# Kernel tuning notes

Hardware: AMD Instinct MI355X
Metric: run time of the kernel (lower is better)

## Reference

```python
import jax, jax.numpy as jnp
import numpy as np

H = 256  # hidden_dim
N = 100000  # num nodes in local_embedding
U = 65536  # num unary clauses
B = 65536  # num binary clauses


def setup_inputs() -> dict:
    key = jax.random.key(0)
    ks = jax.random.split(key, 20)
    s = 0.02
    inp = {
        "local_embedding": jax.random.normal(ks[0], (N, H), dtype=jnp.float32),
        "global_embedding": jax.random.normal(ks[1], (1, H), dtype=jnp.float32),
        "unary_idx": jax.random.randint(ks[2], (U, 2), 0, N, dtype=jnp.int64),
        "binary_idx": jax.random.randint(ks[3], (B, 3), 0, N, dtype=jnp.int64),
        # binary_op_layer: Linear(3H,2H) -> ReLU -> Linear(2H,H)
        "Wb1": jax.random.normal(ks[4], (3 * H, 2 * H), dtype=jnp.float32) * s,
        "bb1": jnp.zeros((2 * H,), dtype=jnp.float32),
        "Wb2": jax.random.normal(ks[5], (2 * H, H), dtype=jnp.float32) * s,
        "bb2": jnp.zeros((H,), dtype=jnp.float32),
        # ternary_op_layer: Linear(4H,2H) -> ReLU -> Linear(2H,H)
        "Wt1": jax.random.normal(ks[6], (4 * H, 2 * H), dtype=jnp.float32) * s,
        "bt1": jnp.zeros((2 * H,), dtype=jnp.float32),
        "Wt2": jax.random.normal(ks[7], (2 * H, H), dtype=jnp.float32) * s,
        "bt2": jnp.zeros((H,), dtype=jnp.float32),
        # common_layer: ReLU -> Linear(H,H) -> ReLU -> Linear(H,1)
        "Wc1": jax.random.normal(ks[8], (H, H), dtype=jnp.float32) * s,
        "bc1": jnp.zeros((H,), dtype=jnp.float32),
        "Wc2": jax.random.normal(ks[9], (H, 1), dtype=jnp.float32) * s,
        "bc2": jnp.zeros((1,), dtype=jnp.float32),
    }
    return inp


def _mlp_branch(rep, W1, b1, W2, b2, Wc1, bc1, Wc2, bc2):
    # op layer: Linear -> ReLU -> Linear
    h = jax.nn.relu(rep @ W1 + b1) @ W2 + b2  # [M, H]
    # common layer: ReLU -> Linear -> ReLU -> Linear(H,1)
    h = jax.nn.relu(jax.nn.relu(h) @ Wc1 + bc1) @ Wc2 + bc2  # [M, 1]
    return h[:, 0]


def reference(local_embedding, global_embedding, unary_idx, binary_idx,
              Wb1, bb1, Wb2, bb2, Wt1, bt1, Wt2, bt2, Wc1, bc1, Wc2, bc2):
    u = unary_idx.shape[0]
    b = binary_idx.shape[0]
    h = global_embedding.shape[-1]
    # gather [U,2,H] node embeddings, append global -> [U,3,H] -> [U,3H]
    g_u = jnp.broadcast_to(global_embedding[None, :, :], (u, 1, h))
    unary_rep = jnp.concatenate(
        (local_embedding[unary_idx, :], g_u), axis=1).reshape(u, 3 * h)
    x_u = _mlp_branch(unary_rep, Wb1, bb1, Wb2, bb2, Wc1, bc1, Wc2, bc2)
    # gather [B,3,H], append global -> [B,4,H] -> [B,4H]
    g_b = jnp.broadcast_to(global_embedding[None, :, :], (b, 1, h))
    binary_rep = jnp.concatenate(
        (local_embedding[binary_idx, :], g_b), axis=1).reshape(b, 4 * h)
    x_b = _mlp_branch(binary_rep, Wt1, bt1, Wt2, bt2, Wc1, bc1, Wc2, bc2)
    x = jnp.concatenate((x_u, x_b))
    return x.reshape(1, x.shape[-1])
```

## Files before the change

### kernel.cpp

```cpp
#include <hip/hip_runtime.h>
#include <cstdint>
#include <cstddef>

typedef __attribute__((ext_vector_type(8))) short s16x8;
typedef __attribute__((ext_vector_type(4))) float fx4;

#define AS1 __attribute__((address_space(1)))
#define AS3 __attribute__((address_space(3)))

__device__ __forceinline__ unsigned short f2bf(float f) {
    union { float f; unsigned u; } c; c.f = f;
    unsigned lsb = (c.u >> 16) & 1u;
    unsigned r = c.u + 0x7fffu + lsb;
    return (unsigned short)(r >> 16);
}

__global__ __launch_bounds__(256) void conv4(const float* __restrict__ src,
                                             unsigned short* __restrict__ dst, int n4) {
    int i = blockIdx.x * 256 + threadIdx.x;
    if (i >= n4) return;
    float4 v = reinterpret_cast<const float4*>(src)[i];
    ushort4 o;
    o.x = f2bf(v.x); o.y = f2bf(v.y); o.z = f2bf(v.z); o.w = f2bf(v.w);
    reinterpret_cast<ushort4*>(dst)[i] = o;
}

__global__ __launch_bounds__(256) void convT(const float* __restrict__ W,
                                             unsigned short* __restrict__ WT, int K, int N) {
    int i = blockIdx.x * 256 + threadIdx.x;
    if (i >= N * K) return;
    int n = i / K, k = i - n * K;
    WT[i] = f2bf(W[(size_t)k * N + n]);
}

__global__ __launch_bounds__(64) void foldbias(const float* __restrict__ g,
                                               const float* __restrict__ W1,
                                               const float* __restrict__ b1,
                                               float* __restrict__ bout,
                                               int K0, int N) {
    int n = blockIdx.x;
    int lane = threadIdx.x;
    float s = 0.f;
#pragma unroll
    for (int j = 0; j < 4; ++j) {
        int k = lane + j * 64;
        s += g[k] * W1[(size_t)(K0 + k) * N + n];
    }
#pragma unroll
    for (int off = 32; off > 0; off >>= 1) s += __shfl_xor(s, off, 64);
    if (lane == 0) bout[n] = b1[n] + s;
}


#define GLL(src, dst) __builtin_amdgcn_global_load_lds((AS1 void*)(src), (AS3 void*)(dst), 16, 0, 0)

#define MFMA16(mh, nh, BARR) do { \
    _Pragma("unroll") for (int ks_ = 0; ks_ < 2; ++ks_) \
    _Pragma("unroll") for (int r_ = 0; r_ < 4; ++r_) \
    _Pragma("unroll") for (int c_ = 0; c_ < 2; ++c_) \
        acc[(mh) * 4 + r_][(nh) * 2 + c_] = __builtin_amdgcn_mfma_f32_16x16x32_bf16( \
            a[r_ * 2 + ks_], BARR[c_ * 2 + ks_], acc[(mh) * 4 + r_][(nh) * 2 + c_], 0, 0, 0); \
} while (0)

#define SYNC_PRE() do { \
    __builtin_amdgcn_s_barrier(); \
    asm volatile("s_waitcnt lgkmcnt(0)" ::: "memory"); \
    __builtin_amdgcn_sched_barrier(0); \
    __builtin_amdgcn_s_setprio(1); \
} while (0)

#define READ_A_AT(basep, mh) do { \
    const char* base_ = (basep); \
    _Pragma("unroll") for (int r_ = 0; r_ < 4; ++r_) { \
        a[r_ * 2 + 0] = *(const s16x8*)(base_ + ((mh) * 4 + r_) * 2048 + c0); \
        a[r_ * 2 + 1] = *(const s16x8*)(base_ + ((mh) * 4 + r_) * 2048 + c1); \
    } \
} while (0)

#define READ_B_AT(basep, nh, BARR) do { \
    const char* base_ = (basep); \
    _Pragma("unroll") for (int c_ = 0; c_ < 2; ++c_) { \
        BARR[c_ * 2 + 0] = *(const s16x8*)(base_ + ((nh) * 2 + c_) * 2048 + c0); \
        BARR[c_ * 2 + 1] = *(const s16x8*)(base_ + ((nh) * 2 + c_) * 2048 + c1); \
    } \
} while (0)

template <int MODE, int K, int NODES>
__global__ __launch_bounds__(512, 2) void gemm256(
    const unsigned short* __restrict__ Abase,
    const int* __restrict__ idx,
    const unsigned short* __restrict__ WT,
    const float* __restrict__ bias,
    unsigned short* __restrict__ Hout,
    int N, int nbn) {
    __shared__ alignas(16) char smem_c[131072];
    constexpr int KT = K / 64;

    const int t = threadIdx.x;
    const int w = t >> 6, lane = t & 63;
    const int wm = w >> 2, wn = w & 3;

    const int nwg = gridDim.x, o = blockIdx.x, q = nwg >> 3;
    const int widx = (o & 7) * q + (o >> 3);
    const int bn = widx % nbn, bm = widx / nbn;

    const int l3 = lane >> 3, l7 = lane & 7, l15 = lane & 15;
    const int scs = (l7 ^ l3) << 4;

    const char* Abc = (const char*)Abase;
    const char* WTc = (const char*)WT;

    uint32_t boff[2][2];
    uint32_t aoff[2][2][NODES];
#pragma unroll
    for (int h = 0; h < 2; ++h)
#pragma unroll
        for (int r = 0; r < 2; ++r) {
            int srow = h * 128 + w * 8 + l3 + r * 64;
            boff[h][r] = (uint32_t)(bn * 256 + srow) * (uint32_t)(K * 2) + scs;
            int gm = bm * 256 + srow;
            if constexpr (MODE == 0) {
                aoff[h][r][0] = (uint32_t)gm * (uint32_t)(K * 2) + scs;
            } else {
#pragma unroll
                for (int s = 0; s < NODES; ++s)
                    aoff[h][r][s] = (uint32_t)idx[(size_t)gm * NODES + s] * 512u + scs;
            }
        }

#define STAGE_A(hh, tsrc, pb) do { \
    char* d_ = smem_c + (pb) * 65536 + (hh) * 16384 + (w << 10); \
    if constexpr (MODE == 0) { \
        GLL(Abc + aoff[hh][0][0] + (tsrc) * 128, d_); \
        GLL(Abc + aoff[hh][1][0] + (tsrc) * 128, d_ + 8192); \
    } else { \
        int seg_ = (tsrc) >> 2, k4_ = ((tsrc) & 3) << 7; \
        uint32_t v0_ = aoff[hh][0][0], v1_ = aoff[hh][1][0]; \
        if constexpr (NODES >= 2) { if (seg_ >= 1) { v0_ = aoff[hh][0][1]; v1_ = aoff[hh][1][1]; } } \
        if constexpr (NODES >= 3) { if (seg_ >= 2) { v0_ = aoff[hh][0][2]; v1_ = aoff[hh][1][2]; } } \
        GLL(Abc + v0_ + k4_, d_); GLL(Abc + v1_ + k4_, d_ + 8192); \
    } \
} while (0)

#define STAGE_B(hh, tsrc, pb) do { \
    char* d_ = smem_c + (pb) * 65536 + 32768 + (hh) * 16384 + (w << 10); \
    GLL(WTc + boff[hh][0] + (tsrc) * 128, d_); \
    GLL(WTc + boff[hh][1] + (tsrc) * 128, d_ + 8192); \
} while (0)

    const int armul = wm * 16384 + l15 * 128;
    const int brmul = 32768 + wn * 8192 + l15 * 128;
    const int hi = (lane >> 4) << 4, xl = l7 << 4;
    const int c0 = hi ^ xl, c1 = (64 + hi) ^ xl;

    fx4 acc[8][4];
#pragma unroll
    for (int i = 0; i < 8; ++i)
#pragma unroll
        for (int j = 0; j < 4; ++j) acc[i][j] = {0.f, 0.f, 0.f, 0.f};

    STAGE_A(0, 0, 0); STAGE_A(1, 0, 0); STAGE_B(0, 0, 0); STAGE_B(1, 0, 0);
    STAGE_A(0, 1, 1);
    asm volatile("s_waitcnt vmcnt(2)" ::: "memory");
    __builtin_amdgcn_s_barrier();

    s16x8 a[8], bl[4], bh[4];
    for (int tt = 0; tt < KT; tt += 2) {
        const int t1 = tt + 1;
        const int t2c = (tt + 2 < KT) ? tt + 2 : KT - 1;
        const int t3c = (tt + 3 < KT) ? tt + 3 : KT - 1;

        READ_A_AT(smem_c + armul, 0); READ_B_AT(smem_c + brmul, 0, bl);
        STAGE_A(1, t1, 1);
        SYNC_PRE(); MFMA16(0, 0, bl); __builtin_amdgcn_s_setprio(0);
        __builtin_amdgcn_s_barrier();

        READ_B_AT(smem_c + brmul, 1, bh);
        STAGE_B(0, t1, 1);
        SYNC_PRE(); MFMA16(0, 1, bh); __builtin_amdgcn_s_setprio(0);
        __builtin_amdgcn_s_barrier();

        READ_A_AT(smem_c + armul, 1);
        STAGE_B(1, t1, 1);
        SYNC_PRE(); MFMA16(1, 0, bl); __builtin_amdgcn_s_setprio(0);
        __builtin_amdgcn_s_barrier();

        STAGE_A(0, t2c, 0);
        SYNC_PRE(); MFMA16(1, 1, bh); __builtin_amdgcn_s_setprio(0);
        asm volatile("s_waitcnt vmcnt(2)" ::: "memory");
        __builtin_amdgcn_s_barrier();

        READ_A_AT(smem_c + 65536 + armul, 0); READ_B_AT(smem_c + 65536 + brmul, 0, bl);
        STAGE_A(1, t2c, 0);
        SYNC_PRE(); MFMA16(0, 0, bl); __builtin_amdgcn_s_setprio(0);
        __builtin_amdgcn_s_barrier();

        READ_B_AT(smem_c + 65536 + brmul, 1, bh);
        STAGE_B(0, t2c, 0);
        SYNC_PRE(); MFMA16(0, 1, bh); __builtin_amdgcn_s_setprio(0);
        __builtin_amdgcn_s_barrier();

        READ_A_AT(smem_c + 65536 + armul, 1);
        STAGE_B(1, t2c, 0);
        SYNC_PRE(); MFMA16(1, 0, bl); __builtin_amdgcn_s_setprio(0);
        __builtin_amdgcn_s_barrier();

        STAGE_A(0, t3c, 1);
        SYNC_PRE(); MFMA16(1, 1, bh); __builtin_amdgcn_s_setprio(0);
        asm volatile("s_waitcnt vmcnt(2)" ::: "memory");
        __builtin_amdgcn_s_barrier();
    }
    asm volatile("s_waitcnt vmcnt(0)" ::: "memory");
#undef STAGE_A
#undef STAGE_B

    const int hi2 = (lane >> 4);
#pragma unroll
    for (int mi = 0; mi < 8; ++mi) {
#pragma unroll
        for (int ni = 0; ni < 4; ++ni) {
            int gcol = bn * 256 + wn * 64 + ni * 16 + l15;
            float bvv = bias[gcol];
            int grow0 = bm * 256 + wm * 128 + mi * 16 + hi2 * 4;
            fx4 v = acc[mi][ni];
#pragma unroll
            for (int j = 0; j < 4; ++j) {
                float x = fmaxf(v[j] + bvv, 0.f);
                Hout[(size_t)(grow0 + j) * N + gcol] = f2bf(x);
            }
        }
    }
}

__global__ __launch_bounds__(512, 2) void gemm_tail(
    const unsigned short* __restrict__ h1,
    const unsigned short* __restrict__ W2T,
    const float* __restrict__ bias2,
    const unsigned short* __restrict__ Wc1T,
    const float* __restrict__ bc1,
    const float* __restrict__ Wc2,
    const float* __restrict__ bc2,
    float* __restrict__ outF) {
    __shared__ alignas(16) char smem_c[163840];
    constexpr int K = 512, KT = K / 64;

    const int t = threadIdx.x;
    const int w = t >> 6, lane = t & 63;
    const int wm = w >> 2, wn = w & 3;
    const int bm = blockIdx.x;

    const int l3 = lane >> 3, l7 = lane & 7, l15 = lane & 15;
    const int scs = (l7 ^ l3) << 4;

    const char* Abc = (const char*)h1;
    const char* WTc = (const char*)W2T;
    const char* Wc1c = (const char*)Wc1T;

    uint32_t boff[2][2], aoff[2][2], c2off[4];
#pragma unroll
    for (int h = 0; h < 2; ++h)
#pragma unroll
        for (int r = 0; r < 2; ++r) {
            int srow = h * 128 + w * 8 + l3 + r * 64;
            boff[h][r] = (uint32_t)srow * (uint32_t)(K * 2) + scs;
            aoff[h][r] = (uint32_t)(bm * 256 + srow) * (uint32_t)(K * 2) + scs;
        }
#pragma unroll
    for (int r = 0; r < 4; ++r) {
        int srow = w * 8 + l3 + r * 64;
        c2off[r] = (uint32_t)srow * 512u + scs;
    }

#define TSTAGE_A(hh, tsrc, pb) do { \
    char* d_ = smem_c + (pb) * 65536 + (hh) * 16384 + (w << 10); \
    GLL(Abc + aoff[hh][0] + (tsrc) * 128, d_); \
    GLL(Abc + aoff[hh][1] + (tsrc) * 128, d_ + 8192); \
} while (0)

#define TSTAGE_B(hh, tsrc, pb) do { \
    char* d_ = smem_c + (pb) * 65536 + 32768 + (hh) * 16384 + (w << 10); \
    GLL(WTc + boff[hh][0] + (tsrc) * 128, d_); \
    GLL(WTc + boff[hh][1] + (tsrc) * 128, d_ + 8192); \
} while (0)

    const int armul = wm * 16384 + l15 * 128;
    const int brmul = 32768 + wn * 8192 + l15 * 128;
    const int hi = (lane >> 4) << 4, xl = l7 << 4;
    const int c0 = hi ^ xl, c1 = (64 + hi) ^ xl;

    fx4 acc[8][4];
#pragma unroll
    for (int i = 0; i < 8; ++i)
#pragma unroll
        for (int j = 0; j < 4; ++j) acc[i][j] = {0.f, 0.f, 0.f, 0.f};

    TSTAGE_A(0, 0, 0); TSTAGE_A(1, 0, 0); TSTAGE_B(0, 0, 0); TSTAGE_B(1, 0, 0);
    TSTAGE_A(0, 1, 1);
    asm volatile("s_waitcnt vmcnt(2)" ::: "memory");
    __builtin_amdgcn_s_barrier();

    s16x8 a[8], bl[4], bh[4];
    for (int tt = 0; tt < KT; tt += 2) {
        const int t1 = tt + 1;
        const int t2c = (tt + 2 < KT) ? tt + 2 : KT - 1;
        const int t3c = (tt + 3 < KT) ? tt + 3 : KT - 1;

        READ_A_AT(smem_c + armul, 0); READ_B_AT(smem_c + brmul, 0, bl);
        TSTAGE_A(1, t1, 1);
        SYNC_PRE(); MFMA16(0, 0, bl); __builtin_amdgcn_s_setprio(0);
        __builtin_amdgcn_s_barrier();

        READ_B_AT(smem_c + brmul, 1, bh);
        TSTAGE_B(0, t1, 1);
        SYNC_PRE(); MFMA16(0, 1, bh); __builtin_amdgcn_s_setprio(0);
        __builtin_amdgcn_s_barrier();

        READ_A_AT(smem_c + armul, 1);
        TSTAGE_B(1, t1, 1);
        SYNC_PRE(); MFMA16(1, 0, bl); __builtin_amdgcn_s_setprio(0);
        __builtin_amdgcn_s_barrier();

        TSTAGE_A(0, t2c, 0);
        SYNC_PRE(); MFMA16(1, 1, bh); __builtin_amdgcn_s_setprio(0);
        asm volatile("s_waitcnt vmcnt(2)" ::: "memory");
        __builtin_amdgcn_s_barrier();

        READ_A_AT(smem_c + 65536 + armul, 0); READ_B_AT(smem_c + 65536 + brmul, 0, bl);
        TSTAGE_A(1, t2c, 0);
        SYNC_PRE(); MFMA16(0, 0, bl); __builtin_amdgcn_s_setprio(0);
        __builtin_amdgcn_s_barrier();

        READ_B_AT(smem_c + 65536 + brmul, 1, bh);
        TSTAGE_B(0, t2c, 0);
        SYNC_PRE(); MFMA16(0, 1, bh); __builtin_amdgcn_s_setprio(0);
        __builtin_amdgcn_s_barrier();

        READ_A_AT(smem_c + 65536 + armul, 1);
        TSTAGE_B(1, t2c, 0);
        SYNC_PRE(); MFMA16(1, 0, bl); __builtin_amdgcn_s_setprio(0);
        __builtin_amdgcn_s_barrier();

        TSTAGE_A(0, t3c, 1);
        SYNC_PRE(); MFMA16(1, 1, bh); __builtin_amdgcn_s_setprio(0);
        asm volatile("s_waitcnt vmcnt(2)" ::: "memory");
        __builtin_amdgcn_s_barrier();
    }
    asm volatile("s_waitcnt vmcnt(0)" ::: "memory");
#undef TSTAGE_A
#undef TSTAGE_B

    __syncthreads();
    const int hi2 = (lane >> 4);
    {
        float b2v[4];
#pragma unroll
        for (int ni = 0; ni < 4; ++ni) b2v[ni] = bias2[wn * 64 + ni * 16 + l15];
#pragma unroll
        for (int mi = 0; mi < 8; ++mi) {
#pragma unroll
            for (int ni = 0; ni < 4; ++ni) {
                int kin2 = (ni * 16 + l15) * 2;
                fx4 v = acc[mi][ni];
#pragma unroll
                for (int j = 0; j < 4; ++j) {
                    int row = wm * 128 + mi * 16 + hi2 * 4 + j;
                    int byte = wn * 32768 + row * 128 + (kin2 ^ ((row & 7) << 4));
                    *(unsigned short*)(smem_c + byte) =
                        f2bf(fmaxf(v[j] + b2v[ni], 0.f));
                }
            }
        }
    }
#pragma unroll
    for (int i = 0; i < 8; ++i)
#pragma unroll
        for (int j = 0; j < 4; ++j) acc[i][j] = {0.f, 0.f, 0.f, 0.f};
    __syncthreads();

    const int brmul2 = 131072 + wn * 8192 + l15 * 128;
    for (int kt = 0; kt < 4; ++kt) {
#pragma unroll
        for (int r = 0; r < 4; ++r)
            GLL(Wc1c + c2off[r] + kt * 128, smem_c + 131072 + r * 8192 + (w << 10));
        asm volatile("s_waitcnt vmcnt(0)" ::: "memory");
        __builtin_amdgcn_s_barrier();

        const char* Abase2 = smem_c + kt * 32768 + armul;
        READ_A_AT(Abase2, 0);
        READ_B_AT(smem_c + brmul2 - 131072 + 131072, 0, bl);
        READ_B_AT(smem_c + brmul2, 1, bh);
        asm volatile("s_waitcnt lgkmcnt(0)" ::: "memory");
        __builtin_amdgcn_sched_barrier(0);
        MFMA16(0, 0, bl); MFMA16(0, 1, bh);
        READ_A_AT(Abase2, 1);
        asm volatile("s_waitcnt lgkmcnt(0)" ::: "memory");
        __builtin_amdgcn_sched_barrier(0);
        MFMA16(1, 0, bl); MFMA16(1, 1, bh);
        __builtin_amdgcn_s_barrier();
    }

    float* part = (float*)(smem_c + 131072);
    float bv[4], wv[4];
#pragma unroll
    for (int ni = 0; ni < 4; ++ni) {
        int gcol = wn * 64 + ni * 16 + l15;
        bv[ni] = bc1[gcol];
        wv[ni] = Wc2[gcol];
    }
#pragma unroll
    for (int mi = 0; mi < 8; ++mi) {
#pragma unroll
        for (int j = 0; j < 4; ++j) {
            float s = 0.f;
#pragma unroll
            for (int ni = 0; ni < 4; ++ni)
                s += fmaxf(acc[mi][ni][j] + bv[ni], 0.f) * wv[ni];
            s += __shfl_xor(s, 1); s += __shfl_xor(s, 2);
            s += __shfl_xor(s, 4); s += __shfl_xor(s, 8);
            if (l15 == 0) {
                int row = wm * 128 + mi * 16 + hi2 * 4 + j;
                part[row * 4 + wn] = s;
            }
        }
    }
    __syncthreads();
    if (t < 256) {
        float o2 = part[t * 4] + part[t * 4 + 1] + part[t * 4 + 2] + part[t * 4 + 3] + bc2[0];
        outF[bm * 256 + t] = o2;
    }
}

extern "C" void kernel_launch(void* const* d_in, const int* in_sizes, int n_in,
                              void* d_out, int out_size, void* d_ws, size_t ws_size,
                              hipStream_t stream) {
    const float* local_emb  = (const float*)d_in[0];
    const float* global_emb = (const float*)d_in[1];
    const int* unary_idx    = (const int*)d_in[2];
    const int* binary_idx   = (const int*)d_in[3];
    const float* Wb1 = (const float*)d_in[4];
    const float* bb1 = (const float*)d_in[5];
    const float* Wb2 = (const float*)d_in[6];
    const float* bb2 = (const float*)d_in[7];
    const float* Wt1 = (const float*)d_in[8];
    const float* bt1 = (const float*)d_in[9];
    const float* Wt2 = (const float*)d_in[10];
    const float* bt2 = (const float*)d_in[11];
    const float* Wc1 = (const float*)d_in[12];
    const float* bc1 = (const float*)d_in[13];
    const float* Wc2 = (const float*)d_in[14];
    const float* bc2 = (const float*)d_in[15];
    float* out = (float*)d_out;

    constexpr int Hd = 256, U = 65536, B = 65536;
    const int NN = in_sizes[0] / Hd;

    char* ws = (char*)d_ws;
    size_t off = 0;
    auto alloc = [&](size_t bytes) {
        char* p = ws + off;
        off += (bytes + 255) & ~(size_t)255;
        return p;
    };
    unsigned short* emb_bf = (unsigned short*)alloc((size_t)NN * Hd * 2);
    unsigned short* W1uT   = (unsigned short*)alloc(512 * 512 * 2);
    unsigned short* W2uT   = (unsigned short*)alloc(256 * 512 * 2);
    unsigned short* W1bT   = (unsigned short*)alloc(512 * 768 * 2);
    unsigned short* W2bT   = (unsigned short*)alloc(256 * 512 * 2);
    unsigned short* Wc1T   = (unsigned short*)alloc(256 * 256 * 2);
    float* bu              = (float*)alloc(512 * 4);
    float* bbn             = (float*)alloc(512 * 4);
    unsigned short* h1     = (unsigned short*)alloc((size_t)U * 512 * 2);

    int n4 = NN * Hd / 4;
    conv4<<<(n4 + 255) / 256, 256, 0, stream>>>(local_emb, emb_bf, n4);
    convT<<<(512 * 512 + 255) / 256, 256, 0, stream>>>(Wb1, W1uT, 512, 512);
    convT<<<(256 * 512 + 255) / 256, 256, 0, stream>>>(Wb2, W2uT, 512, 256);
    convT<<<(512 * 768 + 255) / 256, 256, 0, stream>>>(Wt1, W1bT, 768, 512);
    convT<<<(256 * 512 + 255) / 256, 256, 0, stream>>>(Wt2, W2bT, 512, 256);
    convT<<<(256 * 256 + 255) / 256, 256, 0, stream>>>(Wc1, Wc1T, 256, 256);
    foldbias<<<512, 64, 0, stream>>>(global_emb, Wb1, bb1, bu, 512, 512);
    foldbias<<<512, 64, 0, stream>>>(global_emb, Wt1, bt1, bbn, 768, 512);

    dim3 blk(512);
    gemm256<1, 512, 2><<<dim3(512), blk, 0, stream>>>(
        emb_bf, unary_idx, W1uT, bu, h1, 512, 2);
    gemm_tail<<<dim3(256), blk, 0, stream>>>(h1, W2uT, bb2, Wc1T, bc1, Wc2, bc2, out);
    gemm256<2, 768, 3><<<dim3(512), blk, 0, stream>>>(
        emb_bf, binary_idx, W1bT, bbn, h1, 512, 2);
    gemm_tail<<<dim3(256), blk, 0, stream>>>(h1, W2bT, bt2, Wc1T, bc1, Wc2, bc2, out + U);

    (void)n_in; (void)out_size; (void)ws_size;
}
```

Before: 232.7 us.

## Fuse prep kernels, merge both tail GEMMs into one launch, double-buffer Wc1 staging

Eight small preprocessing launches (embedding bf16 conversion, weight transposes, bias folding) become a single prep kernel that dispatches on block index. The unary and binary first-layer outputs go to separate buffers, so one gemm_tail launch of 512 blocks handles both branches instead of two serialized 256-block launches. The Wc1 stage inside gemm_tail becomes an 8-step double-buffered pipeline with a new swizzled layout, prefetching the next k-slice while the MFMAs run. This trades an extra 64MB h1 workspace buffer for fewer launches and better occupancy of the tail.

```diff
diff --git a/kernel.cpp b/kernel.cpp
--- a/kernel.cpp
+++ b/kernel.cpp
@@ -15,40 +15,62 @@
     return (unsigned short)(r >> 16);
 }
 
-__global__ __launch_bounds__(256) void conv4(const float* __restrict__ src,
-                                             unsigned short* __restrict__ dst, int n4) {
-    int i = blockIdx.x * 256 + threadIdx.x;
-    if (i >= n4) return;
-    float4 v = reinterpret_cast<const float4*>(src)[i];
-    ushort4 o;
-    o.x = f2bf(v.x); o.y = f2bf(v.y); o.z = f2bf(v.z); o.w = f2bf(v.w);
-    reinterpret_cast<ushort4*>(dst)[i] = o;
-}
-
-__global__ __launch_bounds__(256) void convT(const float* __restrict__ W,
-                                             unsigned short* __restrict__ WT, int K, int N) {
-    int i = blockIdx.x * 256 + threadIdx.x;
-    if (i >= N * K) return;
+__device__ __forceinline__ void ctj(const float* __restrict__ W,
+                                    unsigned short* __restrict__ WT,
+                                    int K, int N, int brel, int tid) {
+    int i = brel * 256 + tid;
     int n = i / K, k = i - n * K;
     WT[i] = f2bf(W[(size_t)k * N + n]);
 }
 
-__global__ __launch_bounds__(64) void foldbias(const float* __restrict__ g,
-                                               const float* __restrict__ W1,
-                                               const float* __restrict__ b1,
-                                               float* __restrict__ bout,
-                                               int K0, int N) {
-    int n = blockIdx.x;
-    int lane = threadIdx.x;
+__global__ __launch_bounds__(256) void prep(
+    const float* __restrict__ emb, unsigned short* __restrict__ emb_bf,
+    int n4, int NB1,
+    const float* __restrict__ Wb1, unsigned short* __restrict__ W1uT,
+    const float* __restrict__ Wb2, unsigned short* __restrict__ W2uT,
+    const float* __restrict__ Wt1, unsigned short* __restrict__ W1bT,
+    const float* __restrict__ Wt2, unsigned short* __restrict__ W2bT,
+    const float* __restrict__ Wc1, unsigned short* __restrict__ Wc1T,
+    const float* __restrict__ g, const float* __restrict__ bb1,
+    const float* __restrict__ bt1,
+    float* __restrict__ bu, float* __restrict__ bbn) {
+    int bid = blockIdx.x, tid = threadIdx.x;
+    if (bid < NB1) {
+        int i = bid * 256 + tid;
+        if (i < n4) {
+            float4 v = reinterpret_cast<const float4*>(emb)[i];
+            ushort4 o;
+            o.x = f2bf(v.x); o.y = f2bf(v.y); o.z = f2bf(v.z); o.w = f2bf(v.w);
+            reinterpret_cast<ushort4*>(emb_bf)[i] = o;
+        }
+        return;
+    }
+    int b2 = bid - NB1;
+    if (b2 < 3840) {
+        if (b2 < 1024)      ctj(Wb1, W1uT, 512, 512, b2, tid);
+        else if (b2 < 1536) ctj(Wb2, W2uT, 512, 256, b2 - 1024, tid);
+        else if (b2 < 3072) ctj(Wt1, W1bT, 768, 512, b2 - 1536, tid);
+        else if (b2 < 3584) ctj(Wt2, W2bT, 512, 256, b2 - 3072, tid);
+        else                ctj(Wc1, Wc1T, 256, 256, b2 - 3584, tid);
+        return;
+    }
+    int b3 = b2 - 3840;
+    int wv = tid >> 6, lane = tid & 63;
+    int col = b3 * 4 + wv;
+    const float* W  = (col < 512) ? Wb1 : Wt1;
+    const float* bs = (col < 512) ? bb1 : bt1;
+    float* dst      = (col < 512) ? bu  : bbn;
+    int K0          = (col < 512) ? 512 : 768;
+    int n = col & 511;
     float s = 0.f;
 #pragma unroll
     for (int j = 0; j < 4; ++j) {
         int k = lane + j * 64;
-        s += g[k] * W1[(size_t)(K0 + k) * N + n];
+        s += g[k] * W[(size_t)(K0 + k) * 512 + n];
     }
 #pragma unroll
     for (int off = 32; off > 0; off >>= 1) s += __shfl_xor(s, off, 64);
-    if (lane == 0) bout[n] = b1[n] + s;
+    if (lane == 0) dst[n] = bs[n] + s;
 }
 
 
@@ -233,21 +255,30 @@
 }
 
 __global__ __launch_bounds__(512, 2) void gemm_tail(
-    const unsigned short* __restrict__ h1,
-    const unsigned short* __restrict__ W2T,
-    const float* __restrict__ bias2,
+    const unsigned short* __restrict__ h1u,
+    const unsigned short* __restrict__ h1b,
+    const unsigned short* __restrict__ W2uT,
+    const unsigned short* __restrict__ W2bT,
+    const float* __restrict__ bb2,
+    const float* __restrict__ bt2,
     const unsigned short* __restrict__ Wc1T,
     const float* __restrict__ bc1,
     const float* __restrict__ Wc2,
     const float* __restrict__ bc2,
-    float* __restrict__ outF) {
+    float* __restrict__ outF, int U) {
     __shared__ alignas(16) char smem_c[163840];
     constexpr int K = 512, KT = K / 64;
 
     const int t = threadIdx.x;
     const int w = t >> 6, lane = t & 63;
     const int wm = w >> 2, wn = w & 3;
-    const int bm = blockIdx.x;
+    const int br = blockIdx.x & 1;
+    const int bm = blockIdx.x >> 1;
+
+    const unsigned short* h1  = br ? h1b : h1u;
+    const unsigned short* W2T = br ? W2bT : W2uT;
+    const float* bias2        = br ? bt2 : bb2;
+    float* outp               = outF + br * U;
 
     const int l3 = lane >> 3, l7 = lane & 7, l15 = lane & 15;
     const int scs = (l7 ^ l3) << 4;
@@ -256,7 +287,7 @@
     const char* WTc = (const char*)W2T;
     const char* Wc1c = (const char*)Wc1T;
 
-    uint32_t boff[2][2], aoff[2][2], c2off[4];
+    uint32_t boff[2][2], aoff[2][2];
 #pragma unroll
     for (int h = 0; h < 2; ++h)
 #pragma unroll
@@ -265,10 +296,16 @@
             boff[h][r] = (uint32_t)srow * (uint32_t)(K * 2) + scs;
             aoff[h][r] = (uint32_t)(bm * 256 + srow) * (uint32_t)(K * 2) + scs;
         }
-#pragma unroll
-    for (int r = 0; r < 4; ++r) {
-        int srow = w * 8 + l3 + r * 64;
-        c2off[r] = (uint32_t)srow * 512u + scs;
+
+    uint32_t p2src[2], p2dst[2];
+#pragma unroll
+    for (int p = 0; p < 2; ++p) {
+        int o = p * 8192 + t * 16;
+        int l = o >> 7, u = (o >> 4) & 7;
+        int ulog = u ^ (l & 7);
+        int r = 2 * l + (ulog >> 2), gg = ulog & 3;
+        p2src[p] = (uint32_t)r * 512u + (uint32_t)gg * 16u;
+        p2dst[p] = (uint32_t)o;
     }
 
 #define TSTAGE_A(hh, tsrc, pb) do { \
@@ -281,6 +318,12 @@
     char* d_ = smem_c + (pb) * 65536 + 32768 + (hh) * 16384 + (w << 10); \
     GLL(WTc + boff[hh][0] + (tsrc) * 128, d_); \
     GLL(WTc + boff[hh][1] + (tsrc) * 128, d_ + 8192); \
+} while (0)
+
+#define STAGE2(kt, buf) do { \
+    char* d_ = smem_c + 131072 + (buf) * 16384; \
+    GLL(Wc1c + p2src[0] + (kt) * 64, d_ + p2dst[0]); \
+    GLL(Wc1c + p2src[1] + (kt) * 64, d_ + p2dst[1]); \
 } while (0)
 
     const int armul = wm * 16384 + l15 * 128;
@@ -348,6 +391,8 @@
     asm volatile("s_waitcnt vmcnt(0)" ::: "memory");
 #undef TSTAGE_A
 #undef TSTAGE_B
+
+    STAGE2(0, 0); STAGE2(1, 1);
 
     __syncthreads();
     const int hi2 = (lane >> 4);
@@ -377,27 +422,43 @@
         for (int j = 0; j < 4; ++j) acc[i][j] = {0.f, 0.f, 0.f, 0.f};
     __syncthreads();
 
-    const int brmul2 = 131072 + wn * 8192 + l15 * 128;
-    for (int kt = 0; kt < 4; ++kt) {
-#pragma unroll
-        for (int r = 0; r < 4; ++r)
-            GLL(Wc1c + c2off[r] + kt * 128, smem_c + 131072 + r * 8192 + (w << 10));
-        asm volatile("s_waitcnt vmcnt(0)" ::: "memory");
-        __builtin_amdgcn_s_barrier();
-
-        const char* Abase2 = smem_c + kt * 32768 + armul;
-        READ_A_AT(Abase2, 0);
-        READ_B_AT(smem_c + brmul2 - 131072 + 131072, 0, bl);
-        READ_B_AT(smem_c + brmul2, 1, bh);
+    const int g2 = lane >> 4;
+    for (int kt = 0; kt < 8; ++kt) {
+        if (kt < 7) { asm volatile("s_waitcnt vmcnt(2)" ::: "memory"); }
+        else        { asm volatile("s_waitcnt vmcnt(0)" ::: "memory"); }
+        __builtin_amdgcn_s_barrier();
+
+        s16x8 a2[8], b2f[4];
+        const int kc = kt >> 1, half = kt & 1;
+        const int cb = half * 64 + (g2 << 4);
+        const char* ab = smem_c + kc * 32768;
+#pragma unroll
+        for (int m = 0; m < 8; ++m) {
+            int row = wm * 128 + m * 16 + l15;
+            a2[m] = *(const s16x8*)(ab + row * 128 + (cb ^ ((row & 7) << 4)));
+        }
+        const char* bb = smem_c + 131072 + (kt & 1) * 16384;
+#pragma unroll
+        for (int f = 0; f < 4; ++f) {
+            int r = wn * 64 + f * 16 + l15;
+            int l = r >> 1;
+            int u = (((r & 1) << 2) | g2) ^ (l & 7);
+            b2f[f] = *(const s16x8*)(bb + l * 128 + u * 16);
+        }
         asm volatile("s_waitcnt lgkmcnt(0)" ::: "memory");
         __builtin_amdgcn_sched_barrier(0);
-        MFMA16(0, 0, bl); MFMA16(0, 1, bh);
-        READ_A_AT(Abase2, 1);
-        asm volatile("s_waitcnt lgkmcnt(0)" ::: "memory");
-        __builtin_amdgcn_sched_barrier(0);
-        MFMA16(1, 0, bl); MFMA16(1, 1, bh);
-        __builtin_amdgcn_s_barrier();
-    }
+        __builtin_amdgcn_s_barrier();
+        if (kt + 2 < 8) STAGE2(kt + 2, kt & 1);
+        __builtin_amdgcn_s_setprio(1);
+#pragma unroll
+        for (int m = 0; m < 8; ++m)
+#pragma unroll
+            for (int f = 0; f < 4; ++f)
+                acc[m][f] = __builtin_amdgcn_mfma_f32_16x16x32_bf16(
+                    a2[m], b2f[f], acc[m][f], 0, 0, 0);
+        __builtin_amdgcn_s_setprio(0);
+    }
+#undef STAGE2
 
     float* part = (float*)(smem_c + 131072);
     float bv[4], wv[4];
@@ -426,7 +487,7 @@
     __syncthreads();
     if (t < 256) {
         float o2 = part[t * 4] + part[t * 4 + 1] + part[t * 4 + 2] + part[t * 4 + 3] + bc2[0];
-        outF[bm * 256 + t] = o2;
+        outp[bm * 256 + t] = o2;
     }
 }
 
@@ -451,7 +512,7 @@
     const float* bc2 = (const float*)d_in[15];
     float* out = (float*)d_out;
 
-    constexpr int Hd = 256, U = 65536, B = 65536;
+    constexpr int Hd = 256, U = 65536;
     const int NN = in_sizes[0] / Hd;
 
     char* ws = (char*)d_ws;
@@ -469,25 +530,23 @@
     unsigned short* Wc1T   = (unsigned short*)alloc(256 * 256 * 2);
     float* bu              = (float*)alloc(512 * 4);
     float* bbn             = (float*)alloc(512 * 4);
-    unsigned short* h1     = (unsigned short*)alloc((size_t)U * 512 * 2);
-
-    int n4 = NN * Hd / 4;
-    conv4<<<(n4 + 255) / 256, 256, 0, stream>>>(local_emb, emb_bf, n4);
-    convT<<<(512 * 512 + 255) / 256, 256, 0, stream>>>(Wb1, W1uT, 512, 512);
-    convT<<<(256 * 512 + 255) / 256, 256, 0, stream>>>(Wb2, W2uT, 512, 256);
-    convT<<<(512 * 768 + 255) / 256, 256, 0, stream>>>(Wt1, W1bT, 768, 512);
-    convT<<<(256 * 512 + 255) / 256, 256, 0, stream>>>(Wt2, W2bT, 512, 256);
-    convT<<<(256 * 256 + 255) / 256, 256, 0, stream>>>(Wc1, Wc1T, 256, 256);
-    foldbias<<<512, 64, 0, stream>>>(global_emb, Wb1, bb1, bu, 512, 512);
-    foldbias<<<512, 64, 0, stream>>>(global_emb, Wt1, bt1, bbn, 768, 512);
+    unsigned short* h1u    = (unsigned short*)alloc((size_t)U * 512 * 2);
+    unsigned short* h1b    = (unsigned short*)alloc((size_t)U * 512 * 2);
+
+    int n4 = NN * 64;
+    int NB1 = (n4 + 255) / 256;
+    prep<<<dim3(NB1 + 3840 + 256), dim3(256), 0, stream>>>(
+        local_emb, emb_bf, n4, NB1,
+        Wb1, W1uT, Wb2, W2uT, Wt1, W1bT, Wt2, W2bT, Wc1, Wc1T,
+        global_emb, bb1, bt1, bu, bbn);
 
     dim3 blk(512);
     gemm256<1, 512, 2><<<dim3(512), blk, 0, stream>>>(
-        emb_bf, unary_idx, W1uT, bu, h1, 512, 2);
-    gemm_tail<<<dim3(256), blk, 0, stream>>>(h1, W2uT, bb2, Wc1T, bc1, Wc2, bc2, out);
+        emb_bf, unary_idx, W1uT, bu, h1u, 512, 2);
     gemm256<2, 768, 3><<<dim3(512), blk, 0, stream>>>(
-        emb_bf, binary_idx, W1bT, bbn, h1, 512, 2);
-    gemm_tail<<<dim3(256), blk, 0, stream>>>(h1, W2bT, bt2, Wc1T, bc1, Wc2, bc2, out + U);
+        emb_bf, binary_idx, W1bT, bbn, h1b, 512, 2);
+    gemm_tail<<<dim3(512), blk, 0, stream>>>(
+        h1u, h1b, W2uT, W2bT, bb2, bt2, Wc1T, bc1, Wc2, bc2, out, U);
 
     (void)n_in; (void)out_size; (void)ws_size;
 }
```

Measured after the change: 218.8 us, median of 2. -6.0%, faster.
